# Kernel tuning notes

Measured on AMD Instinct MI355X. Metric: run time of the kernel, lower is better.

## Reference

```python
import jax, jax.numpy as jnp
import numpy as np

DIM = 512
NUM_HEADS = 8
HEAD_DIM = DIM // NUM_HEADS
SCALE = HEAD_DIM ** -0.5


def setup_inputs() -> dict:
    key = jax.random.key(0)
    ks = jax.random.split(key, 5)
    B, D, H, W, C = 2, 8, 16, 16, DIM
    x = jax.random.normal(ks[0], (B, D, H, W, C), dtype=jnp.float32)
    # torch Linear params stored as [in, out] so y = x @ W + b
    qkv_w = jax.random.normal(ks[1], (C, 3 * C), dtype=jnp.float32) * (C ** -0.5)
    qkv_b = jax.random.normal(ks[2], (3 * C,), dtype=jnp.float32) * 0.02
    proj_w = jax.random.normal(ks[3], (C, C), dtype=jnp.float32) * (C ** -0.5)
    proj_b = jax.random.normal(ks[4], (C,), dtype=jnp.float32) * 0.02
    return {"x": x, "qkv_w": qkv_w, "qkv_b": qkv_b, "proj_w": proj_w, "proj_b": proj_b}


def reference(x, qkv_w, qkv_b, proj_w, proj_b):
    B, D, H, W, C = x.shape
    N = D * H * W
    x_flat = x.reshape(B, N, C)
    qkv = (x_flat @ qkv_w + qkv_b).reshape(B, N, 3, NUM_HEADS, HEAD_DIM)
    qkv = jnp.transpose(qkv, (2, 0, 3, 1, 4))  # [3, B, h, N, hd]
    q, k, v = qkv[0], qkv[1], qkv[2]
    attn = jnp.einsum('bhnd,bhmd->bhnm', q, k) * SCALE  # [B, h, N, N]
    attn = jnp.clip(attn, -10000.0, 10000.0)
    attn = jax.nn.softmax(attn, axis=-1)
    attn = jnp.nan_to_num(attn, nan=0.0)
    out = jnp.einsum('bhnm,bhmd->bhnd', attn, v)  # [B, h, N, hd]
    out = jnp.transpose(out, (0, 2, 1, 3)).reshape(B, N, C)
    out = out @ proj_w + proj_b
    return out.reshape(B, D, H, W, C)
```

## Files before the change

### kernel.cpp

```cpp
#include <hip/hip_runtime.h>
#include <stdint.h>

typedef unsigned short u16;
typedef __bf16 bf16x8 __attribute__((ext_vector_type(8)));
typedef _Float16 f16x4 __attribute__((ext_vector_type(4)));
typedef _Float16 f16x8 __attribute__((ext_vector_type(8)));
typedef float  f32x4  __attribute__((ext_vector_type(4)));

__device__ __forceinline__ u16 f2bf(float f) {
  union { float f; unsigned u; } v; v.f = f;
  unsigned r = v.u + 0x7FFFu + ((v.u >> 16) & 1u);
  return (u16)(r >> 16);
}

__device__ __forceinline__ void gload16(const void* g, void* l) {
  __builtin_amdgcn_global_load_lds((const __attribute__((address_space(1))) unsigned int*)g,
                                   (__attribute__((address_space(3))) unsigned int*)l, 16, 0, 0);
}

__device__ __forceinline__ f32x4 mfma32(bf16x8 a, bf16x8 b, f32x4 c) {
  return __builtin_amdgcn_mfma_f32_16x16x32_bf16(a, b, c, 0, 0, 0);
}

__global__ void k_prep(const float* __restrict__ x, const float* __restrict__ qw,
                       const float* __restrict__ pjw, u16* __restrict__ Xb,
                       u16* __restrict__ Wt, u16* __restrict__ Pt) {
  __shared__ u16 tile[64][65];
  const int b = blockIdx.x, t = threadIdx.x;
  if (b < 2048) {
    int i = b * 256 + t;
    float4 v = ((const float4*)x)[i];
    uint2 o;
    o.x = (unsigned)f2bf(v.x) | ((unsigned)f2bf(v.y) << 16);
    o.y = (unsigned)f2bf(v.z) | ((unsigned)f2bf(v.w) << 16);
    ((uint2*)Xb)[i] = o;
    return;
  }
  const float* in; u16* out; int Cc, bx, by;
  if (b < 2240) { in = qw;  out = Wt; Cc = 1536; bx = (b - 2048) % 24; by = (b - 2048) / 24; }
  else          { in = pjw; out = Pt; Cc = 512;  bx = (b - 2240) & 7;  by = (b - 2240) >> 3; }
  const int c0 = bx * 64, r0 = by * 64;
  #pragma unroll
  for (int i = 0; i < 16; ++i) {
    int idx = t + i * 256;
    int r = idx >> 6, c = idx & 63;
    tile[c][r] = f2bf(in[(size_t)(r0 + r) * Cc + c0 + c]);
  }
  __syncthreads();
  #pragma unroll
  for (int i = 0; i < 16; ++i) {
    int idx = t + i * 256;
    int r = idx >> 6, c = idx & 63;
    out[(size_t)(c0 + r) * 512 + r0 + c] = tile[r][c];
  }
}

__device__ __forceinline__ int swz64(int row, int colByte) {
  return (row * 128 + (colByte ^ ((row & 7) << 4))) >> 1;
}
__device__ __forceinline__ int swzK(int row, int colByte) {
  return (row * 128 + (colByte ^ ((row & 3) << 4) ^ (((row >> 3) & 1) << 6))) >> 1;
}

template<int BM, int BN>
__device__ __forceinline__ void gemm_core(const u16* __restrict__ A, const u16* __restrict__ Bt,
                                          int m0, int n0, f32x4 (&acc)[BM/32][BN/32],
                                          u16* lA, u16* lB) {
  const int t = threadIdx.x;
  const int lane = t & 63;
  const int w = t >> 6, wr = w >> 1, wc = w & 1;
  const int lr = lane & 15, lg = lane >> 4;
  const int r0 = t >> 3, j0 = t & 7;
  const int cA = (j0 ^ (r0 & 7)) * 8;
  #pragma unroll 1
  for (int k0 = 0; k0 < 512; k0 += 64) {
    __syncthreads();
    #pragma unroll
    for (int u = 0; u < BM / 32; ++u)
      gload16(A + (size_t)(m0 + u * 32 + r0) * 512 + k0 + cA, (char*)lA + u * 4096 + w * 1024);
    #pragma unroll
    for (int u = 0; u < BN / 32; ++u)
      gload16(Bt + (size_t)(n0 + u * 32 + r0) * 512 + k0 + cA, (char*)lB + u * 4096 + w * 1024);
    __syncthreads();
    #pragma unroll
    for (int kh = 0; kh < 2; ++kh) {
      bf16x8 af[BM / 32], bfr[BN / 32];
      #pragma unroll
      for (int i = 0; i < BM / 32; ++i)
        af[i] = __builtin_bit_cast(bf16x8, *(const uint4*)&lA[swz64(wr * (BM / 2) + i * 16 + lr, kh * 64 + lg * 16)]);
      #pragma unroll
      for (int j = 0; j < BN / 32; ++j)
        bfr[j] = __builtin_bit_cast(bf16x8, *(const uint4*)&lB[swz64(wc * (BN / 2) + j * 16 + lr, kh * 64 + lg * 16)]);
      #pragma unroll
      for (int i = 0; i < BM / 32; ++i)
        #pragma unroll
        for (int j = 0; j < BN / 32; ++j)
          acc[i][j] = mfma32(af[i], bfr[j], acc[i][j]);
    }
  }
}

__global__ __launch_bounds__(256, 2) void k_gemm_qkv(const u16* __restrict__ A, const u16* __restrict__ Bt,
                                                     const float* __restrict__ bias,
                                                     u16* __restrict__ Qb, u16* __restrict__ Kb,
                                                     u16* __restrict__ Vtb) {
  __shared__ __align__(16) u16 lA[128 * 64];
  __shared__ __align__(16) u16 lB[64 * 64];
  __shared__ __align__(16) u16 vt[9216];
  f32x4 acc[4][2];
  #pragma unroll
  for (int i = 0; i < 4; ++i)
    #pragma unroll
    for (int j = 0; j < 2; ++j) acc[i][j] = (f32x4){0.f, 0.f, 0.f, 0.f};
  const int m0 = blockIdx.x * 128, n0 = blockIdx.y * 64;
  gemm_core<128, 64>(A, Bt, m0, n0, acc, lA, lB);
  const int t = threadIdx.x;
  const int lane = t & 63;
  const int w = t >> 6, wr = w >> 1, wc = w & 1;
  const int lr = lane & 15, lg = lane >> 4;
  const int which = n0 >> 9, h = (n0 >> 6) & 7;
  const int b = m0 >> 11, m0l = m0 & 2047;
  const size_t bh = (size_t)(b * 8 + h);
  if (which != 2) {
    const float scl = (which == 0) ? 0.18033688011112042f : 1.0f;
    #pragma unroll
    for (int i = 0; i < 4; ++i)
      #pragma unroll
      for (int j = 0; j < 2; ++j) {
        int n = n0 + wc * 32 + j * 16 + lr;
        float bb = bias[n];
        #pragma unroll
        for (int r = 0; r < 4; ++r)
          vt[(wr * 64 + i * 16 + lg * 4 + r) * 72 + wc * 32 + j * 16 + lr] =
              f2bf((acc[i][j][r] + bb) * scl);
      }
    __syncthreads();
    u16* dst = (which == 0 ? Qb : Kb) + (bh * 2048 + m0l) * 64;
    #pragma unroll
    for (int it = 0; it < 4; ++it) {
      int unit = it * 256 + t, row = unit >> 3, ch = unit & 7;
      *(uint4*)&dst[row * 64 + ch * 8] = *(const uint4*)&vt[row * 72 + ch * 8];
    }
  } else {
    #pragma unroll
    for (int i = 0; i < 4; ++i)
      #pragma unroll
      for (int j = 0; j < 2; ++j) {
        int n = n0 + wc * 32 + j * 16 + lr;
        float bb = bias[n];
        uint2 pk;
        pk.x = (unsigned)f2bf(acc[i][j][0] + bb) | ((unsigned)f2bf(acc[i][j][1] + bb) << 16);
        pk.y = (unsigned)f2bf(acc[i][j][2] + bb) | ((unsigned)f2bf(acc[i][j][3] + bb) << 16);
        *(uint2*)&vt[(wc * 32 + j * 16 + lr) * 136 + wr * 64 + i * 16 + lg * 4] = pk;
      }
    __syncthreads();
    u16* dst = Vtb + bh * 64 * 2048 + m0l;
    #pragma unroll
    for (int it = 0; it < 4; ++it) {
      int unit = it * 256 + t, row = unit >> 4, ch = unit & 15;
      *(uint4*)&dst[(size_t)row * 2048 + ch * 8] = *(const uint4*)&vt[row * 136 + ch * 8];
    }
  }
}

__global__ __launch_bounds__(256, 2) void k_gemm_proj(const u16* __restrict__ A, const u16* __restrict__ Bt,
                                                      const float* __restrict__ bias,
                                                      float* __restrict__ out) {
  __shared__ __align__(16) u16 lA[64 * 64];
  __shared__ __align__(16) u16 lB[64 * 64];
  f32x4 acc[2][2];
  #pragma unroll
  for (int i = 0; i < 2; ++i)
    #pragma unroll
    for (int j = 0; j < 2; ++j) acc[i][j] = (f32x4){0.f, 0.f, 0.f, 0.f};
  const int m0 = blockIdx.x * 64, n0 = blockIdx.y * 64;
  gemm_core<64, 64>(A, Bt, m0, n0, acc, lA, lB);
  const int lane = threadIdx.x & 63;
  const int w = threadIdx.x >> 6, wr = w >> 1, wc = w & 1;
  const int lr = lane & 15, lg = lane >> 4;
  #pragma unroll
  for (int i = 0; i < 2; ++i)
    #pragma unroll
    for (int j = 0; j < 2; ++j)
      #pragma unroll
      for (int r = 0; r < 4; ++r) {
        int m = m0 + wr * 32 + i * 16 + lg * 4 + r;
        int n = n0 + wc * 32 + j * 16 + lr;
        out[(size_t)m * 512 + n] = acc[i][j][r] + bias[n];
      }
}

__global__ __launch_bounds__(512, 4) void k_attn(const u16* __restrict__ Qb, const u16* __restrict__ Kb,
                                                 const u16* __restrict__ Vtb,
                                                 u16* __restrict__ Op, float* __restrict__ Lp) {
  __shared__ __align__(16) u16 smem[18432];
  u16* Kt0 = smem;
  u16* Kt1 = smem + 4096;
  u16* Vl0 = smem + 8192;
  u16* Vl1 = smem + 12288;
  const int t = threadIdx.x;
  const int lane = t & 63, w = t >> 6;
  const int lr = lane & 15, lg = lane >> 4;
  const int f = blockIdx.x;
  const int xc = f & 7, jj = f >> 3;
  const int group = xc + ((jj >> 3) << 3);
  const int qtile = jj & 7, bh = group & 15, split = group >> 4;
  const int q0 = qtile * 256 + w * 32;
  const int sBeg = split * 512;

  bf16x8 qf[2][2];
  #pragma unroll
  for (int c = 0; c < 2; ++c) {
    const u16* qrow = Qb + ((size_t)bh * 2048 + q0 + c * 16 + lr) * 64;
    qf[c][0] = __builtin_bit_cast(bf16x8, *(const uint4*)(qrow + lg * 8));
    qf[c][1] = __builtin_bit_cast(bf16x8, *(const uint4*)(qrow + 32 + lg * 8));
  }

  f32x4 oacc[2][4], lacc[2];
  #pragma unroll
  for (int c = 0; c < 2; ++c) {
    lacc[c] = (f32x4){0.f, 0.f, 0.f, 0.f};
    #pragma unroll
    for (int ff = 0; ff < 4; ++ff) oacc[c][ff] = (f32x4){0.f, 0.f, 0.f, 0.f};
  }
  bf16x8 ones8;
  #pragma unroll
  for (int k = 0; k < 8; ++k) ones8[k] = (__bf16)1.f;
  const f32x4 NEG12 = (f32x4){-12.f, -12.f, -12.f, -12.f};

  const int prowBase = ((lr >> 2) << 3) + (lr & 3);

  const int r0 = t >> 3, j0 = t & 7;
  const int cK = (j0 ^ ((r0 & 3) | (((r0 >> 3) & 1) << 2))) * 8;
  const int cV = (j0 ^ (r0 & 7)) * 8;
  const u16* Kbase = Kb + (size_t)bh * 2048 * 64;
  const u16* Vbase = Vtb + (size_t)bh * 64 * 2048;
  const u16* kg0 = Kbase + (size_t)(sBeg + r0) * 64 + cK;
  const u16* vg0 = Vbase + (size_t)r0 * 2048 + sBeg + cV;

  gload16(kg0, Kt0 + w * 512);
  gload16(vg0, Vl0 + w * 512);
  kg0 += 4096; vg0 += 64;

  auto TILE = [&](u16* KC, u16* VC, u16* KN, u16* VN) {
    __syncthreads();
    gload16(kg0, KN + w * 512);
    gload16(vg0, VN + w * 512);
    kg0 += 4096; vg0 += 64;
    #pragma unroll
    for (int j32 = 0; j32 < 2; ++j32) {
      f32x4 sa[2][2];
      __builtin_amdgcn_s_setprio(1);
      #pragma unroll
      for (int p = 0; p < 2; ++p) {
        const int prow = j32 * 32 + p * 4 + prowBase;
        bf16x8 kb0 = __builtin_bit_cast(bf16x8, *(const uint4*)&KC[swzK(prow, lg * 16)]);
        bf16x8 kb1 = __builtin_bit_cast(bf16x8, *(const uint4*)&KC[swzK(prow, 64 + lg * 16)]);
        #pragma unroll
        for (int c = 0; c < 2; ++c) {
          f32x4 z = mfma32(kb0, qf[c][0], NEG12);
          sa[c][p] = mfma32(kb1, qf[c][1], z);
        }
      }
      __builtin_amdgcn_s_setprio(0);
      bf16x8 pb[2];
      #pragma unroll
      for (int c = 0; c < 2; ++c)
        #pragma unroll
        for (int p = 0; p < 2; ++p)
          #pragma unroll
          for (int r = 0; r < 4; ++r)
            pb[c][p * 4 + r] = (__bf16)exp2f(sa[c][p][r]);
      __builtin_amdgcn_s_setprio(1);
      lacc[0] = mfma32(ones8, pb[0], lacc[0]);
      lacc[1] = mfma32(ones8, pb[1], lacc[1]);
      #pragma unroll
      for (int ff = 0; ff < 4; ++ff) {
        bf16x8 va = __builtin_bit_cast(bf16x8, *(const uint4*)&VC[swz64(ff * 16 + lr, j32 * 64 + lg * 16)]);
        oacc[0][ff] = mfma32(va, pb[0], oacc[0][ff]);
        oacc[1][ff] = mfma32(va, pb[1], oacc[1][ff]);
      }
      __builtin_amdgcn_s_setprio(0);
    }
  };

  #pragma unroll 1
  for (int tt = 0; tt < 4; ++tt) {
    TILE(Kt0, Vl0, Kt1, Vl1);
    TILE(Kt1, Vl1, Kt0, Vl0);
  }

  __syncthreads();
  #pragma unroll
  for (int c = 0; c < 2; ++c) {
    const int ql = w * 32 + c * 16 + lr;
    #pragma unroll
    for (int ff = 0; ff < 4; ++ff) {
      f16x4 hv;
      hv[0] = (_Float16)oacc[c][ff][0]; hv[1] = (_Float16)oacc[c][ff][1];
      hv[2] = (_Float16)oacc[c][ff][2]; hv[3] = (_Float16)oacc[c][ff][3];
      *(uint2*)&smem[ql * 72 + ff * 16 + lg * 4] = __builtin_bit_cast(uint2, hv);
    }
  }
  __syncthreads();
  {
    u16* dst = Op + ((size_t)(split * 16 + bh) * 2048 + qtile * 256) * 64;
    #pragma unroll
    for (int it = 0; it < 4; ++it) {
      int unit = it * 512 + t, row = unit >> 3, ch = unit & 7;
      *(uint4*)&dst[row * 64 + ch * 8] = *(const uint4*)&smem[row * 72 + ch * 8];
    }
  }
  #pragma unroll
  for (int c = 0; c < 2; ++c) {
    if (lg == 0) {
      const size_t orow = (size_t)((split * 16 + bh) * 2048) + q0 + c * 16 + lr;
      Lp[orow] = lacc[c][0];
    }
  }
}

__global__ void k_combine(const u16* __restrict__ Op, const float* __restrict__ Lp,
                          u16* __restrict__ AO) {
  int idx = blockIdx.x * 256 + threadIdx.x;
  int chunk = idx & 7, row = idx >> 3;
  float den = Lp[row] + Lp[32768 + row] + Lp[65536 + row] + Lp[98304 + row];
  float inv = 1.0f / den;
  float o[8];
  #pragma unroll
  for (int k = 0; k < 8; ++k) o[k] = 0.f;
  #pragma unroll
  for (int s = 0; s < 4; ++s) {
    uint4 u = ((const uint4*)Op)[(size_t)s * 262144 + row * 8 + chunk];
    f16x8 hv = __builtin_bit_cast(f16x8, u);
    #pragma unroll
    for (int k = 0; k < 8; ++k) o[k] += (float)hv[k];
  }
  bf16x8 bv;
  #pragma unroll
  for (int k = 0; k < 8; ++k) bv[k] = (__bf16)(o[k] * inv);
  int bh = row >> 11, q = row & 2047, bb = bh >> 3, h = bh & 7;
  *(uint4*)&AO[((size_t)(bb * 2048 + q)) * 512 + h * 64 + chunk * 8] = __builtin_bit_cast(uint4, bv);
}

extern "C" void kernel_launch(void* const* d_in, const int* in_sizes, int n_in,
                              void* d_out, int out_size, void* d_ws, size_t ws_size,
                              hipStream_t stream) {
  (void)in_sizes; (void)n_in; (void)out_size; (void)ws_size;
  const float* x      = (const float*)d_in[0];
  const float* qkv_w  = (const float*)d_in[1];
  const float* qkv_b  = (const float*)d_in[2];
  const float* proj_w = (const float*)d_in[3];
  const float* proj_b = (const float*)d_in[4];
  float* out = (float*)d_out;
  char* wsc = (char*)d_ws;
  float* Lp  = (float*)(wsc + 0);
  u16*   Xb  = (u16*)(wsc + 0);
  u16*   Wt  = (u16*)(wsc + 4194304);
  u16*   Pt  = (u16*)(wsc + 5767168);
  u16*   Qb  = (u16*)(wsc + 6291456);
  u16*   Kb  = (u16*)(wsc + 10485760);
  u16*   Vtb = (u16*)(wsc + 14680064);
  u16*   AO  = (u16*)(wsc + 18874368);
  u16*   Op  = (u16*)(wsc + 23068672);

  k_prep<<<2304, 256, 0, stream>>>(x, qkv_w, proj_w, Xb, Wt, Pt);
  k_gemm_qkv<<<dim3(32, 24), 256, 0, stream>>>(Xb, Wt, qkv_b, Qb, Kb, Vtb);
  k_attn<<<512, 512, 0, stream>>>(Qb, Kb, Vtb, Op, Lp);
  k_combine<<<1024, 256, 0, stream>>>(Op, Lp, AO);
  k_gemm_proj<<<dim3(64, 8), 256, 0, stream>>>(AO, Pt, proj_b, out);
}
```

Before: 60.32 us.

## Stage two K/V tiles per barrier in a four-slot LDS ring

Moves the attention kernel's K/V staging from a two-slot ping-pong with a barrier per 64-key tile to a four-slot ring. Two tiles are loaded ahead and two are computed per __syncthreads. This halves the barriers and deepens prefetch to hide global-to-LDS latency. LDS use grows from about 36KB to 64KB per block, which may cut blocks per CU against the launch bound of 4. The epilogue still reuses smem after a sync, so results should be unchanged.

```diff
diff --git a/kernel.cpp b/kernel.cpp
--- a/kernel.cpp
+++ b/kernel.cpp
@@ -193,11 +193,7 @@
 __global__ __launch_bounds__(512, 4) void k_attn(const u16* __restrict__ Qb, const u16* __restrict__ Kb,
                                                  const u16* __restrict__ Vtb,
                                                  u16* __restrict__ Op, float* __restrict__ Lp) {
-  __shared__ __align__(16) u16 smem[18432];
-  u16* Kt0 = smem;
-  u16* Kt1 = smem + 4096;
-  u16* Vl0 = smem + 8192;
-  u16* Vl1 = smem + 12288;
+  __shared__ __align__(16) u16 smem[32768];
   const int t = threadIdx.x;
   const int lane = t & 63, w = t >> 6;
   const int lr = lane & 15, lg = lane >> 4;
@@ -235,18 +231,18 @@
   const int cV = (j0 ^ (r0 & 7)) * 8;
   const u16* Kbase = Kb + (size_t)bh * 2048 * 64;
   const u16* Vbase = Vtb + (size_t)bh * 64 * 2048;
-  const u16* kg0 = Kbase + (size_t)(sBeg + r0) * 64 + cK;
-  const u16* vg0 = Vbase + (size_t)r0 * 2048 + sBeg + cV;
-
-  gload16(kg0, Kt0 + w * 512);
-  gload16(vg0, Vl0 + w * 512);
-  kg0 += 4096; vg0 += 64;
-
-  auto TILE = [&](u16* KC, u16* VC, u16* KN, u16* VN) {
-    __syncthreads();
-    gload16(kg0, KN + w * 512);
-    gload16(vg0, VN + w * 512);
-    kg0 += 4096; vg0 += 64;
+  const u16* kg = Kbase + (size_t)(sBeg + r0) * 64 + cK;
+  const u16* vg = Vbase + (size_t)r0 * 2048 + sBeg + cV;
+
+  auto STAGE = [&](int slot) {
+    gload16(kg, smem + slot * 4096 + w * 512);
+    gload16(vg, smem + 16384 + slot * 4096 + w * 512);
+    kg += 4096; vg += 64;
+  };
+
+  auto COMPUTE = [&](int slot) {
+    const u16* KC = smem + slot * 4096;
+    const u16* VC = smem + 16384 + slot * 4096;
     #pragma unroll
     for (int j32 = 0; j32 < 2; ++j32) {
       f32x4 sa[2][2];
@@ -284,10 +280,14 @@
     }
   };
 
+  STAGE(0); STAGE(1);
   #pragma unroll 1
-  for (int tt = 0; tt < 4; ++tt) {
-    TILE(Kt0, Vl0, Kt1, Vl1);
-    TILE(Kt1, Vl1, Kt0, Vl0);
+  for (int pp = 0; pp < 4; ++pp) {
+    const int sA = (pp & 1) * 2;
+    __syncthreads();
+    if (pp < 3) { STAGE(sA ^ 2); STAGE((sA ^ 2) + 1); }
+    COMPUTE(sA);
+    COMPUTE(sA + 1);
   }
 
   __syncthreads();
```

Result: no change. 60.64 us (+0.5%).
